# Kernel tuning notes

Hardware: AMD Instinct MI355X
Metric: run time of the kernel (lower is better)

Reference implementation:

```python
import jax, jax.numpy as jnp
import numpy as np

B, H, W_SP, C_IN, C_OUT = 8, 256, 256, 64, 64
MODES = (32, 32)
M1, M2 = MODES[0], MODES[1] // 2 + 1  # weight_modes = [32, 17]


def setup_inputs() -> dict:
    key = jax.random.key(0)
    k1, k2, k3 = jax.random.split(key, 3)
    scale = 1.0 / C_IN
    x = jax.random.normal(k1, (B, H, W_SP, C_IN), dtype=jnp.float32)
    W_real = scale * jax.random.normal(k2, (M1, M2, C_IN, C_OUT), dtype=jnp.float32)
    W_imag = scale * jax.random.normal(k3, (M1, M2, C_IN, C_OUT), dtype=jnp.float32)
    return {"x": x, "W_real": W_real, "W_imag": W_imag}


def reference(x, W_real, W_imag):
    # x: [B, H, W, C_in] (channels last, as in the torch module)
    b, h, w, c_in = x.shape
    m1, m2, _, c_out = W_real.shape
    # permute(0, -1, 1, 2) -> channels first
    xc = jnp.transpose(x, (0, 3, 1, 2))  # [B, C_in, H, W]
    # rfftn over the two spatial dims, norm='forward'
    spec = jnp.fft.rfftn(xc, axes=(-2, -1), norm='forward')  # [B, C_in, H, W//2+1]
    # fftshift over all spectral dims except the last (rfft) dim
    spec_sh = jnp.fft.fftshift(spec, axes=(-2,))
    # _compute_spectrum_slices: starts = [H - m1, (W//2+1) - m2]
    start1 = h - m1
    r0 = start1 // 2  # slice(start//2, -start//2) on fftshifted axis
    xs = spec_sh[:, :, r0:r0 + m1, :m2]  # [B, C_in, m1, m2]
    # multiplier: per-mode complex linear map over channels (channels-last call)
    Wc = (W_real + 1j * W_imag).astype(spec.dtype)  # [m1, m2, C_in, C_out]
    conv_modes = jnp.einsum('bimn,mnio->bomn', xs, Wc)  # [B, C_out, m1, m2]
    # scatter into a full-size zero spectrum, then undo the shift
    conv = jnp.zeros((b, c_out, h, w // 2 + 1), dtype=spec.dtype)
    conv = conv.at[:, :, r0:r0 + m1, :m2].set(conv_modes)
    conv = jnp.fft.ifftshift(conv, axes=(-2,))
    # inverse rfftn back to the original spatial grid
    y = jnp.fft.irfftn(conv, s=(h, w), axes=(-2, -1), norm='forward')  # [B, C_out, H, W]
    # permute(0, 2, 3, 1) -> channels last
    return jnp.transpose(y, (0, 2, 3, 1))
```

## Files before the change

kernel.cpp:

```cpp
#include <hip/hip_runtime.h>


#define NB 8
#define NH 256
#define NW 256
#define NC 64
#define NM1 32
#define NM2 17
#define HQ 4

__global__ void k0_tw(float* __restrict__ twD, float* __restrict__ twB,
                      float* __restrict__ twC) {
    const float STEP = 0.02454369260617026f;
    int t = blockIdx.x * 256 + threadIdx.x;
    if (t < 64 * 18) {
        int w = t / 18, nn = t % 18;
        if (nn < 17) {
            int ph = (nn * w) & 255;
            float ang = (float)ph * STEP;
            twD[w * 36 + 2 * nn + 0] = cosf(ang);
            twD[w * 36 + 2 * nn + 1] = sinf(ang);
        } else {
            twD[w * 36 + 34] = 0.f;
            twD[w * 36 + 35] = 0.f;
        }
    }
    if (t < 256 * 32) {
        int h = t >> 5, m = t & 31;
        int ph = ((m - 16) * h) & 255;
        float ang = (float)ph * STEP;
        twB[t * 2 + 0] = cosf(ang);
        twB[t * 2 + 1] = sinf(ang);
    }
    if (t < 17) {
        twC[t] = 2.0f * cosf((float)t * STEP);
    }
}

template <int QP1>
__device__ __forceinline__ void k1_fixup(float* s1a, float* s2a,
                                         float* s1b, float* s2b,
                                         const float* cn, const float* sn) {
    const float R = 0.7071067811865476f;
    const float CR[8] = {1.f,  R, 0.f, -R, -1.f, -R, 0.f,  R};
    const float SI[8] = {0.f, -R, -1.f, -R, 0.f,  R, 1.f,  R};
    #pragma unroll
    for (int n = 0; n < 17; ++n) {
        float qr0 = fmaf(cn[n], s1a[n], -s2a[n]);
        float qi0 = sn[n] * s1a[n];
        float qr1 = fmaf(cn[n], s1b[n], -s2b[n]);
        float qi1 = sn[n] * s1b[n];
        const int k = (n * QP1) & 7;
        float cr = CR[k], si = SI[k];
        s1a[n] = qr0 * cr - qi0 * si;
        s2a[n] = qr0 * si + qi0 * cr;
        s1b[n] = qr1 * cr - qi1 * si;
        s2b[n] = qr1 * si + qi1 * cr;
    }
}

__global__ __launch_bounds__(256) void k1_fwdW(const float* __restrict__ x,
                                               const float* __restrict__ twD,
                                               const float* __restrict__ twC,
                                               float* __restrict__ G) {
    __shared__ float lre[4][17][64];
    __shared__ float lim[4][17][64];
    const int tid = threadIdx.x;
    const int i = tid & 63;
    const int wq_u = __builtin_amdgcn_readfirstlane(tid >> 6);
    const int bh0 = blockIdx.x * 2;

    float twoc[17], cn[17], sn[17];
    #pragma unroll
    for (int n = 0; n < 17; ++n) {
        twoc[n] = twC[n];
        cn[n] = twD[36 + 2 * n];
        sn[n] = twD[36 + 2 * n + 1];
    }

    float s1a[17], s2a[17], s1b[17], s2b[17];
    #pragma unroll
    for (int n = 0; n < 17; ++n) { s1a[n]=0.f; s2a[n]=0.f; s1b[n]=0.f; s2b[n]=0.f; }

    const float* xb0  = x + (size_t)bh0 * (NW * NC) + (size_t)wq_u * 32 * 64 + i;
    const float* xb0c = xb0 + 128 * 64;
    const float* xb1  = xb0 + NW * NC;
    const float* xb1c = xb1 + 128 * 64;
    #pragma unroll 2
    for (int j = 0; j < 32; j += 2) {
        float a0 = xb0 [(size_t)j * 64];
        float a1 = xb0 [(size_t)(j + 1) * 64];
        float c0 = xb0c[(size_t)j * 64];
        float c1 = xb0c[(size_t)(j + 1) * 64];
        float b0 = xb1 [(size_t)j * 64];
        float b1 = xb1 [(size_t)(j + 1) * 64];
        float d0 = xb1c[(size_t)j * 64];
        float d1 = xb1c[(size_t)(j + 1) * 64];
        float u0j = a0 + c0, u0k = a1 + c1;
        float v0j = a0 - c0, v0k = a1 - c1;
        float u1j = b0 + d0, u1k = b1 + d1;
        float v1j = b0 - d0, v1k = b1 - d1;
        #pragma unroll
        for (int n = 0; n < 17; ++n) {
            float in0j = (n & 1) ? v0j : u0j;
            float in0k = (n & 1) ? v0k : u0k;
            float in1j = (n & 1) ? v1j : u1j;
            float in1k = (n & 1) ? v1k : u1k;
            float ta = fmaf(twoc[n], s1a[n], in0j) - s2a[n];
            float tb = fmaf(twoc[n], ta, in0k) - s1a[n];
            s2a[n] = ta; s1a[n] = tb;
            float ua = fmaf(twoc[n], s1b[n], in1j) - s2b[n];
            float ub = fmaf(twoc[n], ua, in1k) - s1b[n];
            s2b[n] = ua; s1b[n] = ub;
        }
    }

    switch (wq_u) {
        case 0:  k1_fixup<1>(s1a, s2a, s1b, s2b, cn, sn); break;
        case 1:  k1_fixup<2>(s1a, s2a, s1b, s2b, cn, sn); break;
        case 2:  k1_fixup<3>(s1a, s2a, s1b, s2b, cn, sn); break;
        default: k1_fixup<4>(s1a, s2a, s1b, s2b, cn, sn); break;
    }

    #pragma unroll
    for (int n = 0; n < 17; ++n) { lre[wq_u][n][i] = s1a[n]; lim[wq_u][n][i] = s2a[n]; }
    __syncthreads();
    float2* G0 = (float2*)G + (size_t)bh0 * 17 * 64;
    for (int n = wq_u; n < 17; n += 4) {
        float re = (lre[0][n][i] + lre[1][n][i]) + (lre[2][n][i] + lre[3][n][i]);
        float im = (lim[0][n][i] + lim[1][n][i]) + (lim[2][n][i] + lim[3][n][i]);
        G0[n * 64 + i] = make_float2(re, im);
    }
    __syncthreads();
    #pragma unroll
    for (int n = 0; n < 17; ++n) { lre[wq_u][n][i] = s1b[n]; lim[wq_u][n][i] = s2b[n]; }
    __syncthreads();
    float2* G1 = G0 + 17 * 64;
    for (int n = wq_u; n < 17; n += 4) {
        float re = (lre[0][n][i] + lre[1][n][i]) + (lre[2][n][i] + lre[3][n][i]);
        float im = (lim[0][n][i] + lim[1][n][i]) + (lim[2][n][i] + lim[3][n][i]);
        G1[n * 64 + i] = make_float2(re, im);
    }
}

__global__ __launch_bounds__(256) void k2a_hdft(const float* __restrict__ G,
                                                const float* __restrict__ twB,
                                                float* __restrict__ P) {
    const int bn = blockIdx.x;
    const int b = bn / 17, n = bn % 17;
    const int hq = blockIdx.y;
    const int t = threadIdx.x;
    const int lane = t & 63;
    const int q_u = __builtin_amdgcn_readfirstlane(t >> 6);

    float ar[8], ai[8];
    #pragma unroll
    for (int j = 0; j < 8; ++j) { ar[j] = 0.f; ai[j] = 0.f; }

    const float2* Gb = (const float2*)G + ((size_t)b * 256 * 17 + n) * 64 + lane;
    #pragma unroll 2
    for (int hh = 0; hh < 64; ++hh) {
        int h = hq * 64 + hh;
        float2 g = Gb[(size_t)h * (17 * 64)];
        const float* tw = twB + (h * 32 + q_u * 8) * 2;
        #pragma unroll
        for (int j = 0; j < 8; ++j) {
            float c = tw[2 * j], s = tw[2 * j + 1];
            ar[j] = fmaf(g.x, c, fmaf(g.y, s, ar[j]));
            ai[j] = fmaf(g.y, c, fmaf(-g.x, s, ai[j]));
        }
    }
    float2* Pp = (float2*)P + (((size_t)hq * 136 + bn) * 32 + q_u * 8) * 64 + lane;
    #pragma unroll
    for (int j = 0; j < 8; ++j) Pp[j * 64] = make_float2(ar[j], ai[j]);
}

__global__ __launch_bounds__(512) void k2b_mix(const float* __restrict__ P,
                                               const float* __restrict__ Wr,
                                               const float* __restrict__ Wi,
                                               float* __restrict__ Z) {
    __shared__ float2 xs[8 * 64];
    const int mn = blockIdx.x;
    const int m = mn & 31, n = mn >> 5;
    const int t = threadIdx.x;
    const int lane = t & 63;
    const int q_u = __builtin_amdgcn_readfirstlane(t >> 6);

    {
        int b = t >> 6, i = t & 63;
        const float2* Pp = (const float2*)P + (((size_t)(b * 17 + n)) * 32 + m) * 64 + i;
        float re = 0.f, im = 0.f;
        #pragma unroll
        for (int hq = 0; hq < HQ; ++hq) {
            float2 pv = Pp[(size_t)hq * (136 * 32 * 64)];
            re += pv.x; im += pv.y;
        }
        xs[t] = make_float2(re, im);
    }
    __syncthreads();

    const float scale = (n == 0 ? 1.0f : 2.0f) * (1.0f / 65536.0f);
    float zr = 0.f, zi = 0.f;
    const float* Wrp = Wr + (((size_t)m * 17 + n) * 64) * 64 + lane;
    const float* Wip = Wi + (((size_t)m * 17 + n) * 64) * 64 + lane;
    #pragma unroll 4
    for (int i = 0; i < 64; ++i) {
        float wr = Wrp[(size_t)i * 64], wi = Wip[(size_t)i * 64];
        float2 xv = xs[q_u * 64 + i];
        zr = fmaf(xv.x, wr, fmaf(-xv.y, wi, zr));
        zi = fmaf(xv.x, wi, fmaf(xv.y, wr, zi));
    }
    float2* Zp = (float2*)Z;
    Zp[(((size_t)q_u * 17 + n) * 32 + m) * 64 + lane] = make_float2(zr * scale, zi * scale);
}

__global__ __launch_bounds__(256) void k2c_ihdft(const float* __restrict__ Z,
                                                 const float* __restrict__ twB,
                                                 float* __restrict__ T) {
    __shared__ float2 zs[32 * 64];
    const int bn = blockIdx.x;
    const int b = bn / 17, n = bn % 17;
    const int hq = blockIdx.y;
    const int t = threadIdx.x;
    const int lane = t & 63;
    const int q_u = __builtin_amdgcn_readfirstlane(t >> 6);

    const float2* Zp = (const float2*)Z + (((size_t)b * 17 + n) * 32) * 64;
    #pragma unroll
    for (int r = 0; r < 8; ++r) zs[r * 256 + t] = Zp[r * 256 + t];
    __syncthreads();

    float2* Tb = (float2*)T + ((size_t)b * 256 * 17 + n) * 64 + lane;
    #pragma unroll 2
    for (int jj = 0; jj < 8; ++jj) {
        int h = hq * 32 + q_u * 8 + jj;
        const float* tw = twB + h * 64;
        float re0 = 0, im0 = 0, re1 = 0, im1 = 0;
        #pragma unroll
        for (int m = 0; m < 32; m += 2) {
            float2 z0 = zs[m * 64 + lane];
            float c0 = tw[2 * m + 0], s0 = tw[2 * m + 1];
            re0 = fmaf(z0.x, c0, fmaf(-z0.y, s0, re0));
            im0 = fmaf(z0.x, s0, fmaf(z0.y, c0, im0));
            float2 z1 = zs[(m + 1) * 64 + lane];
            float c1 = tw[2 * m + 2], s1 = tw[2 * m + 3];
            re1 = fmaf(z1.x, c1, fmaf(-z1.y, s1, re1));
            im1 = fmaf(z1.x, s1, fmaf(z1.y, c1, im1));
        }
        Tb[(size_t)h * (17 * 64)] = make_float2(re0 + re1, im0 + im1);
    }
}

__global__ __launch_bounds__(256) void k3_invW(const float* __restrict__ T,
                                               const float* __restrict__ twD,
                                               float* __restrict__ y) {
    __shared__ float tws[32 * 36];
    const int tid = threadIdx.x;
    const int o = tid & 63;
    const int q_u = __builtin_amdgcn_readfirstlane(tid >> 6);
    const int bh0 = blockIdx.x * 2;
    const float R8 = 0.7071067811865476f;

    {
        const float4* src = (const float4*)twD;
        float4* dst = (float4*)tws;
        #pragma unroll
        for (int v = tid; v < 288; v += 256) dst[v] = src[v];
    }

    const float2* T0 = (const float2*)T + (size_t)bh0 * 17 * 64;
    const float2* T1 = T0 + 17 * 64;
    float tr0[17], ti0[17], tr1[17], ti1[17];
    #pragma unroll
    for (int n = 0; n < 17; ++n) {
        float2 v0 = T0[n * 64 + o];
        tr0[n] = v0.x; ti0[n] = v0.y;
        float2 v1 = T1[n * 64 + o];
        tr1[n] = v1.x; ti1[n] = v1.y;
    }
    __syncthreads();

    float* yb0 = y + (size_t)bh0 * (NW * NC) + o;
    float* yb1 = yb0 + NW * NC;
    #pragma unroll 1
    for (int it = 0; it < 8; ++it) {
        const int wp = q_u * 8 + it;
        const float* tw = &tws[wp * 36];
        float P0a=0,P1a=0,P2a=0,P3a=0,P4a=0,P5a=0,P6a=0,P7a=0;
        float Q1a=0,Q2a=0,Q3a=0,Q5a=0,Q6a=0,Q7a=0;
        float P0b=0,P1b=0,P2b=0,P3b=0,P4b=0,P5b=0,P6b=0,P7b=0;
        float Q1b=0,Q2b=0,Q3b=0,Q5b=0,Q6b=0,Q7b=0;

        #pragma unroll
        for (int n = 0; n < 17; n += 8) {
            float c = tw[2*n], s = tw[2*n+1];
            P0a = fmaf(tr0[n], c, fmaf(-ti0[n], s, P0a));
            P0b = fmaf(tr1[n], c, fmaf(-ti1[n], s, P0b));
        }
        #pragma unroll
        for (int n = 4; n < 17; n += 8) {
            float c = tw[2*n], s = tw[2*n+1];
            P4a = fmaf(tr0[n], c, fmaf(-ti0[n], s, P4a));
            P4b = fmaf(tr1[n], c, fmaf(-ti1[n], s, P4b));
        }
        #pragma unroll
        for (int n = 1; n < 17; n += 8) {
            float c = tw[2*n], s = tw[2*n+1];
            P1a = fmaf(tr0[n], c, fmaf(-ti0[n], s, P1a));
            Q1a = fmaf(tr0[n], s, fmaf( ti0[n], c, Q1a));
            P1b = fmaf(tr1[n], c, fmaf(-ti1[n], s, P1b));
            Q1b = fmaf(tr1[n], s, fmaf( ti1[n], c, Q1b));
        }
        #pragma unroll
        for (int n = 2; n < 17; n += 8) {
            float c = tw[2*n], s = tw[2*n+1];
            P2a = fmaf(tr0[n], c, fmaf(-ti0[n], s, P2a));
            Q2a = fmaf(tr0[n], s, fmaf( ti0[n], c, Q2a));
            P2b = fmaf(tr1[n], c, fmaf(-ti1[n], s, P2b));
            Q2b = fmaf(tr1[n], s, fmaf( ti1[n], c, Q2b));
        }
        #pragma unroll
        for (int n = 3; n < 17; n += 8) {
            float c = tw[2*n], s = tw[2*n+1];
            P3a = fmaf(tr0[n], c, fmaf(-ti0[n], s, P3a));
            Q3a = fmaf(tr0[n], s, fmaf( ti0[n], c, Q3a));
            P3b = fmaf(tr1[n], c, fmaf(-ti1[n], s, P3b));
            Q3b = fmaf(tr1[n], s, fmaf( ti1[n], c, Q3b));
        }
        #pragma unroll
        for (int n = 5; n < 17; n += 8) {
            float c = tw[2*n], s = tw[2*n+1];
            P5a = fmaf(tr0[n], c, fmaf(-ti0[n], s, P5a));
            Q5a = fmaf(tr0[n], s, fmaf( ti0[n], c, Q5a));
            P5b = fmaf(tr1[n], c, fmaf(-ti1[n], s, P5b));
            Q5b = fmaf(tr1[n], s, fmaf( ti1[n], c, Q5b));
        }
        #pragma unroll
        for (int n = 6; n < 17; n += 8) {
            float c = tw[2*n], s = tw[2*n+1];
            P6a = fmaf(tr0[n], c, fmaf(-ti0[n], s, P6a));
            Q6a = fmaf(tr0[n], s, fmaf( ti0[n], c, Q6a));
            P6b = fmaf(tr1[n], c, fmaf(-ti1[n], s, P6b));
            Q6b = fmaf(tr1[n], s, fmaf( ti1[n], c, Q6b));
        }
        #pragma unroll
        for (int n = 7; n < 17; n += 8) {
            float c = tw[2*n], s = tw[2*n+1];
            P7a = fmaf(tr0[n], c, fmaf(-ti0[n], s, P7a));
            Q7a = fmaf(tr0[n], s, fmaf( ti0[n], c, Q7a));
            P7b = fmaf(tr1[n], c, fmaf(-ti1[n], s, P7b));
            Q7b = fmaf(tr1[n], s, fmaf( ti1[n], c, Q7b));
        }

        {
            float Se = (P0a + P2a) + (P4a + P6a);
            float So = (P1a + P3a) + (P5a + P7a);
            float C  = (P0a - P2a) + (P4a - P6a);
            float S  = (Q3a - Q1a) + (Q7a - Q5a);
            float D  = P0a - P4a;
            float Hq = Q2a - Q6a;
            float G1 = (P1a - P3a) - (P5a - P7a);
            float G2 = (Q1a + Q3a) - (Q5a + Q7a);
            float u  = R8 * (G1 - G2);
            float v  = R8 * (G1 + G2);
            float dm = D - Hq, dp = D + Hq;
            yb0[(size_t)(wp +   0) * 64] = Se + So;
            yb0[(size_t)(wp +  32) * 64] = dm + u;
            yb0[(size_t)(wp +  64) * 64] = C + S;
            yb0[(size_t)(wp +  96) * 64] = dp - v;
            yb0[(size_t)(wp + 128) * 64] = Se - So;
            yb0[(size_t)(wp + 160) * 64] = dm - u;
            yb0[(size_t)(wp + 192) * 64] = C - S;
            yb0[(size_t)(wp + 224) * 64] = dp + v;
        }
        {
            float Se = (P0b + P2b) + (P4b + P6b);
            float So = (P1b + P3b) + (P5b + P7b);
            float C  = (P0b - P2b) + (P4b - P6b);
            float S  = (Q3b - Q1b) + (Q7b - Q5b);
            float D  = P0b - P4b;
            float Hq = Q2b - Q6b;
            float G1 = (P1b - P3b) - (P5b - P7b);
            float G2 = (Q1b + Q3b) - (Q5b + Q7b);
            float u  = R8 * (G1 - G2);
            float v  = R8 * (G1 + G2);
            float dm = D - Hq, dp = D + Hq;
            yb1[(size_t)(wp +   0) * 64] = Se + So;
            yb1[(size_t)(wp +  32) * 64] = dm + u;
            yb1[(size_t)(wp +  64) * 64] = C + S;
            yb1[(size_t)(wp +  96) * 64] = dp - v;
            yb1[(size_t)(wp + 128) * 64] = Se - So;
            yb1[(size_t)(wp + 160) * 64] = dm - u;
            yb1[(size_t)(wp + 192) * 64] = C - S;
            yb1[(size_t)(wp + 224) * 64] = dp + v;
        }
    }
}

extern "C" void kernel_launch(void* const* d_in, const int* in_sizes, int n_in,
                              void* d_out, int out_size, void* d_ws, size_t ws_size,
                              hipStream_t stream) {
    (void)in_sizes; (void)n_in; (void)out_size; (void)ws_size;
    const float* x  = (const float*)d_in[0];
    const float* Wr = (const float*)d_in[1];
    const float* Wi = (const float*)d_in[2];
    float* out = (float*)d_out;
    float* ws  = (float*)d_ws;

    float* twD = ws;
    float* twB = ws + 2304;
    float* twC = ws + 18688;
    float* G   = ws + 18720;
    float* T   = G + 4456448;
    float* P   = T;
    float* Z   = G;

    k0_tw<<<32, 256, 0, stream>>>(twD, twB, twC);
    k1_fwdW<<<NB * NH / 2, 256, 0, stream>>>(x, twD, twC, G);
    k2a_hdft<<<dim3(NB * NM2, HQ), 256, 0, stream>>>(G, twB, P);
    k2b_mix<<<NM1 * NM2, 512, 0, stream>>>(P, Wr, Wi, Z);
    k2c_ihdft<<<dim3(NB * NM2, 8), 256, 0, stream>>>(Z, twB, T);
    k3_invW<<<NB * NH / 2, 256, 0, stream>>>(T, twD, out);
}
```

Measured before the change: 130.5 us.

## Exploit twiddle periodicity in inverse H-DFT by splitting modes mod 4

```diff
diff --git a/kernel.cpp b/kernel.cpp
--- a/kernel.cpp
+++ b/kernel.cpp
@@ -218,6 +218,7 @@
                                                  const float* __restrict__ twB,
                                                  float* __restrict__ T) {
     __shared__ float2 zs[32 * 64];
+    __shared__ float tws[8 * 64];
     const int bn = blockIdx.x;
     const int b = bn / 17, n = bn % 17;
     const int hq = blockIdx.y;
@@ -228,26 +229,45 @@
     const float2* Zp = (const float2*)Z + (((size_t)b * 17 + n) * 32) * 64;
     #pragma unroll
     for (int r = 0; r < 8; ++r) zs[r * 256 + t] = Zp[r * 256 + t];
+    if (t < 128) {
+        ((float4*)tws)[t] = ((const float4*)(twB + (size_t)hq * 8 * 64))[t];
+    }
     __syncthreads();
 
     float2* Tb = (float2*)T + ((size_t)b * 256 * 17 + n) * 64 + lane;
-    #pragma unroll 2
-    for (int jj = 0; jj < 8; ++jj) {
-        int h = hq * 32 + q_u * 8 + jj;
-        const float* tw = twB + h * 64;
-        float re0 = 0, im0 = 0, re1 = 0, im1 = 0;
-        #pragma unroll
-        for (int m = 0; m < 32; m += 2) {
-            float2 z0 = zs[m * 64 + lane];
-            float c0 = tw[2 * m + 0], s0 = tw[2 * m + 1];
-            re0 = fmaf(z0.x, c0, fmaf(-z0.y, s0, re0));
-            im0 = fmaf(z0.x, s0, fmaf(z0.y, c0, im0));
+    #pragma unroll
+    for (int jj = 0; jj < 2; ++jj) {
+        const int hl = q_u * 2 + jj;
+        const int hp = hq * 8 + hl;
+        const float* tw = &tws[hl * 64];
+        float A0r=0,A0i=0,A1r=0,A1i=0,A2r=0,A2i=0,A3r=0,A3i=0;
+        #pragma unroll
+        for (int m = 0; m < 32; m += 4) {
+            float2 z0 = zs[(m + 0) * 64 + lane];
+            float c0 = tw[2*m + 0], s0 = tw[2*m + 1];
+            A0r = fmaf(z0.x, c0, fmaf(-z0.y, s0, A0r));
+            A0i = fmaf(z0.x, s0, fmaf( z0.y, c0, A0i));
             float2 z1 = zs[(m + 1) * 64 + lane];
-            float c1 = tw[2 * m + 2], s1 = tw[2 * m + 3];
-            re1 = fmaf(z1.x, c1, fmaf(-z1.y, s1, re1));
-            im1 = fmaf(z1.x, s1, fmaf(z1.y, c1, im1));
-        }
-        Tb[(size_t)h * (17 * 64)] = make_float2(re0 + re1, im0 + im1);
+            float c1 = tw[2*m + 2], s1 = tw[2*m + 3];
+            A1r = fmaf(z1.x, c1, fmaf(-z1.y, s1, A1r));
+            A1i = fmaf(z1.x, s1, fmaf( z1.y, c1, A1i));
+            float2 z2 = zs[(m + 2) * 64 + lane];
+            float c2 = tw[2*m + 4], s2 = tw[2*m + 5];
+            A2r = fmaf(z2.x, c2, fmaf(-z2.y, s2, A2r));
+            A2i = fmaf(z2.x, s2, fmaf( z2.y, c2, A2i));
+            float2 z3 = zs[(m + 3) * 64 + lane];
+            float c3 = tw[2*m + 6], s3 = tw[2*m + 7];
+            A3r = fmaf(z3.x, c3, fmaf(-z3.y, s3, A3r));
+            A3i = fmaf(z3.x, s3, fmaf( z3.y, c3, A3i));
+        }
+        float Er = A0r + A2r, Ei = A0i + A2i;
+        float Fr = A0r - A2r, Fi = A0i - A2i;
+        float Gr = A1r + A3r, Gi = A1i + A3i;
+        float Hr = A1r - A3r, Hi = A1i - A3i;
+        Tb[(size_t)(hp +   0) * (17 * 64)] = make_float2(Er + Gr, Ei + Gi);
+        Tb[(size_t)(hp +  64) * (17 * 64)] = make_float2(Fr - Hi, Fi + Hr);
+        Tb[(size_t)(hp + 128) * (17 * 64)] = make_float2(Er - Gr, Ei - Gi);
+        Tb[(size_t)(hp + 192) * (17 * 64)] = make_float2(Fr + Hi, Fi - Hr);
     }
 }
 
```

New measurement: 116.0 us. 1.13x faster.
